# Optimization experiments

Measured on AMD Instinct MI355X. Metric: run time of the kernel, lower is better.

## Reference

```python
import jax, jax.numpy as jnp
import numpy as np

OFFSETS = (12, 20, 30, 42, 55, 67)  # pixel offsets along shadow direction


def _bilinear_shift(img, dx, dy):
    """Sample img (H,W) at (y+dy, x+dx), bilinear, zero padding.
    Equivalent to F.grid_sample with identity affine_grid + uniform shift
    (align_corners=True): normalized shift d*2/(W-1) == d pixels.
    Separable interpolation (valid because padding is zeros)."""
    H, W = img.shape
    xs = jnp.arange(W, dtype=img.dtype) + dx  # (W,) sample x-coords
    ys = jnp.arange(H, dtype=img.dtype) + dy  # (H,) sample y-coords
    x0f = jnp.floor(xs); wx = xs - x0f
    y0f = jnp.floor(ys); wy = ys - y0f
    x0 = x0f.astype(jnp.int32); x1 = x0 + 1
    y0 = y0f.astype(jnp.int32); y1 = y0 + 1

    def gx(ix):  # gather columns with zero padding
        valid = ((ix >= 0) & (ix < W)).astype(img.dtype)
        return img[:, jnp.clip(ix, 0, W - 1)] * valid[None, :]

    row = gx(x0) * (1.0 - wx)[None, :] + gx(x1) * wx[None, :]  # (H,W)

    def gy(iy):  # gather rows with zero padding
        valid = ((iy >= 0) & (iy < H)).astype(img.dtype)
        return row[jnp.clip(iy, 0, H - 1), :] * valid[:, None]

    return gy(y0) * (1.0 - wy)[:, None] + gy(y1) * wy[:, None]


def _warp_stack(shadow_map, shadow_dir):
    """shadow_map (B,1,H,W), shadow_dir (B,2) -> (B,n_offsets,H,W)."""
    img = shadow_map[:, 0]  # (B,H,W)
    d = jnp.asarray(OFFSETS, dtype=img.dtype)  # (n,)
    dx = shadow_dir[:, 0:1] * d          # (B,n) pixel shift in x
    dy = -shadow_dir[:, 1:2] * d         # (B,n) pixel shift in y
    f = jax.vmap(jax.vmap(_bilinear_shift, in_axes=(None, 0, 0)),
                 in_axes=(0, 0, 0))
    return f(img, dx, dy)  # (B,n,H,W)


def setup_inputs() -> dict:
    key = jax.random.key(0)
    k1, k2, k3, k4, k5 = jax.random.split(key, 5)
    B, C, Hf, Wf = 4, 512, 128, 128
    H, W = 1024, 1024
    n = len(OFFSETS)
    rgb_feat = jax.random.normal(k1, (B, C, Hf, Wf), dtype=jnp.float32)
    shadow_map = jax.random.uniform(k2, (B, 1, H, W), dtype=jnp.float32)
    shadow_dir = jax.random.normal(k3, (B, 2), dtype=jnp.float32)
    shadow_dir = shadow_dir / jnp.linalg.norm(shadow_dir, axis=-1, keepdims=True)
    w_conv = 0.02 * jax.random.normal(k4, (C, n), dtype=jnp.float32)
    b_conv = 0.02 * jax.random.normal(k5, (C,), dtype=jnp.float32)
    gate = jnp.ones((1,), dtype=jnp.float32) * 0.01
    return {"rgb_feat": rgb_feat, "shadow_map": shadow_map,
            "shadow_dir": shadow_dir, "w_conv": w_conv,
            "b_conv": b_conv, "gate": gate}


def reference(rgb_feat, shadow_map, shadow_dir, w_conv, b_conv, gate):
    B, C, Hf, Wf = rgb_feat.shape
    n = len(OFFSETS)
    evidence = _warp_stack(shadow_map, shadow_dir)  # (B,n,H,W)
    # bilinear downsample, align_corners=False, no antialias (matches torch)
    evidence = jax.image.resize(evidence, (B, n, Hf, Wf),
                                method="linear", antialias=False)
    mixed = jnp.einsum("bnhw,cn->bchw", evidence, w_conv) \
            + b_conv[None, :, None, None]
    return rgb_feat + gate[0] * mixed
```

## Files before the change

kernel.cpp:

```cpp
#include <hip/hip_runtime.h>

#define HRES 1024
#define WRES 1024
#define HF   128
#define WF   128
#define NOFF 6
#define CCH  512
#define BB   4
#define CHUNK 32

typedef float vfloat4 __attribute__((ext_vector_type(4)));
typedef vfloat4 uvfloat4 __attribute__((aligned(4)));

__global__ void evidence_kernel(const float* __restrict__ smap,
                                const float* __restrict__ sdir,
                                float* __restrict__ E) {
    int t = blockIdx.x * blockDim.x + threadIdx.x;
    if (t >= BB * NOFF * HF * WF) return;
    int j = t & (WF - 1);
    int i = (t >> 7) & (HF - 1);
    int k = (t >> 14) % NOFF;
    int b = t / (NOFF << 14);

    const float offs[NOFF] = {12.f, 20.f, 30.f, 42.f, 55.f, 67.f};
    float dirx = sdir[b * 2 + 0];
    float diry = sdir[b * 2 + 1];
    float d  = offs[k];
    float dx = dirx * d;
    float dy = -diry * d;
    float fxf = floorf(dx), fyf = floorf(dy);
    float wx = dx - fxf,    wy = dy - fyf;

    int X0 = 8 * j + 3 + (int)fxf;
    int Y0 = 8 * i + 3 + (int)fyf;

    float wx0 = 0.5f * (1.f - wx), wx1 = 0.5f, wx2 = 0.5f * wx;
    float wyv[3] = {0.5f * (1.f - wy), 0.5f, 0.5f * wy};

    const float* img = smap + (size_t)b * HRES * WRES;
    bool fastx = (X0 >= 0) & (X0 + 3 < WRES);
    float acc = 0.f;
#pragma unroll
    for (int r = 0; r < 3; ++r) {
        int y = Y0 + r;
        if ((unsigned)y < HRES) {
            const float* rowp = img + (size_t)y * WRES;
            float s0, s1, s2;
            if (fastx) {
                vfloat4 v = *reinterpret_cast<const uvfloat4*>(rowp + X0);
                s0 = v.x; s1 = v.y; s2 = v.z;
            } else {
                s0 = ((unsigned)(X0 + 0) < WRES) ? rowp[X0 + 0] : 0.f;
                s1 = ((unsigned)(X0 + 1) < WRES) ? rowp[X0 + 1] : 0.f;
                s2 = ((unsigned)(X0 + 2) < WRES) ? rowp[X0 + 2] : 0.f;
            }
            acc += (s0 * wx0 + s1 * wx1 + s2 * wx2) * wyv[r];
        }
    }
    E[t] = acc;
}

__global__ __launch_bounds__(256) void mix_kernel(
        const float* __restrict__ rgb,
        const float* __restrict__ E,
        const float* __restrict__ w_conv,
        const float* __restrict__ b_conv,
        const float* __restrict__ gate,
        float* __restrict__ out) {
    __shared__ float s_w[CHUNK * NOFF];
    __shared__ float s_b[CHUNK];

    int tile = blockIdx.x;
    int b    = tile >> 4;
    int p    = (tile & 15) * 1024 + threadIdx.x * 4;
    int c0   = blockIdx.y * CHUNK;
    float g  = gate[0];

    for (int idx = threadIdx.x; idx < CHUNK * NOFF; idx += blockDim.x)
        s_w[idx] = g * w_conv[(size_t)(c0 + idx / NOFF) * NOFF + idx % NOFF];
    for (int idx = threadIdx.x; idx < CHUNK; idx += blockDim.x)
        s_b[idx] = g * b_conv[c0 + idx];
    __syncthreads();

    vfloat4 e[NOFF];
#pragma unroll
    for (int k = 0; k < NOFF; ++k)
        e[k] = *reinterpret_cast<const vfloat4*>(
            E + (((size_t)(b * NOFF + k)) << 14) + p);

    const vfloat4* rgbp = reinterpret_cast<const vfloat4*>(
        rgb + (((size_t)(b * CCH + c0)) << 14) + p);
    vfloat4* outp = reinterpret_cast<vfloat4*>(
        out + (((size_t)(b * CCH + c0)) << 14) + p);
    const int stride4 = (1 << 14) / 4;

#pragma unroll
    for (int c8 = 0; c8 < CHUNK / 8; ++c8) {
        vfloat4 r[8];
#pragma unroll
        for (int u = 0; u < 8; ++u)
            r[u] = __builtin_nontemporal_load(
                rgbp + (size_t)(c8 * 8 + u) * stride4);
#pragma unroll
        for (int u = 0; u < 8; ++u) {
            int c = c8 * 8 + u;
            float w0 = s_w[c * NOFF + 0], w1 = s_w[c * NOFF + 1];
            float w2 = s_w[c * NOFF + 2], w3 = s_w[c * NOFF + 3];
            float w4 = s_w[c * NOFF + 4], w5 = s_w[c * NOFF + 5];
            float bb = s_b[c];
            vfloat4 o;
            o.x = r[u].x + bb + e[0].x * w0 + e[1].x * w1 + e[2].x * w2
                               + e[3].x * w3 + e[4].x * w4 + e[5].x * w5;
            o.y = r[u].y + bb + e[0].y * w0 + e[1].y * w1 + e[2].y * w2
                               + e[3].y * w3 + e[4].y * w4 + e[5].y * w5;
            o.z = r[u].z + bb + e[0].z * w0 + e[1].z * w1 + e[2].z * w2
                               + e[3].z * w3 + e[4].z * w4 + e[5].z * w5;
            o.w = r[u].w + bb + e[0].w * w0 + e[1].w * w1 + e[2].w * w2
                               + e[3].w * w3 + e[4].w * w4 + e[5].w * w5;
            __builtin_nontemporal_store(o, outp + (size_t)c * stride4);
        }
    }
}

extern "C" void kernel_launch(void* const* d_in, const int* in_sizes, int n_in,
                              void* d_out, int out_size, void* d_ws, size_t ws_size,
                              hipStream_t stream) {
    const float* rgb    = (const float*)d_in[0];
    const float* smap   = (const float*)d_in[1];
    const float* sdir   = (const float*)d_in[2];
    const float* w_conv = (const float*)d_in[3];
    const float* b_conv = (const float*)d_in[4];
    const float* gate   = (const float*)d_in[5];
    float* out = (float*)d_out;

    float* E = (float*)d_ws;
    int n_e = BB * NOFF * HF * WF;
    evidence_kernel<<<(n_e + 255) / 256, 256, 0, stream>>>(smap, sdir, E);

    dim3 grid_mix(BB * 16, CCH / CHUNK);
    mix_kernel<<<grid_mix, 256, 0, stream>>>(rgb, E, w_conv, b_conv, gate, out);
}
```

Before: 58.60 us.

## Remap evidence blocks for locality and drop shared-memory weight staging in mix

The evidence kernel now permutes block indices so that consecutively scheduled blocks work on neighbouring rows of the shadow map, aiming for better L2/cache reuse of the overlapping 3x3 row reads across XCDs. The mix kernel no longer stages gated weights and biases in shared memory behind a barrier. Instead it loads weights directly (scalar/uniform loads) and folds the gate into the evidence values once. This removes the LDS fill and __syncthreads, and the mix kernel is memory-bound on the rgb stream, so the gain is likely small.

```diff
diff --git a/kernel.cpp b/kernel.cpp
--- a/kernel.cpp
+++ b/kernel.cpp
@@ -15,8 +15,15 @@
 __global__ void evidence_kernel(const float* __restrict__ smap,
                                 const float* __restrict__ sdir,
                                 float* __restrict__ E) {
-    int t = blockIdx.x * blockDim.x + threadIdx.x;
-    if (t >= BB * NOFF * HF * WF) return;
+    int B = blockIdx.x;
+    int r   = B & 7;
+    int q   = B >> 3;
+    int b64 = q >> 3;
+    int sub = q & 7;
+    int off = 4 * r + sub + (sub >= 4 ? 28 : 0);
+    int c   = b64 * 64 + off;
+    int t   = c * 256 + threadIdx.x;
+
     int j = t & (WF - 1);
     int i = (t >> 7) & (HF - 1);
     int k = (t >> 14) % NOFF;
@@ -41,8 +48,8 @@
     bool fastx = (X0 >= 0) & (X0 + 3 < WRES);
     float acc = 0.f;
 #pragma unroll
-    for (int r = 0; r < 3; ++r) {
-        int y = Y0 + r;
+    for (int rr = 0; rr < 3; ++rr) {
+        int y = Y0 + rr;
         if ((unsigned)y < HRES) {
             const float* rowp = img + (size_t)y * WRES;
             float s0, s1, s2;
@@ -54,7 +61,7 @@
                 s1 = ((unsigned)(X0 + 1) < WRES) ? rowp[X0 + 1] : 0.f;
                 s2 = ((unsigned)(X0 + 2) < WRES) ? rowp[X0 + 2] : 0.f;
             }
-            acc += (s0 * wx0 + s1 * wx1 + s2 * wx2) * wyv[r];
+            acc += (s0 * wx0 + s1 * wx1 + s2 * wx2) * wyv[rr];
         }
     }
     E[t] = acc;
@@ -67,26 +74,19 @@
         const float* __restrict__ b_conv,
         const float* __restrict__ gate,
         float* __restrict__ out) {
-    __shared__ float s_w[CHUNK * NOFF];
-    __shared__ float s_b[CHUNK];
-
     int tile = blockIdx.x;
     int b    = tile >> 4;
     int p    = (tile & 15) * 1024 + threadIdx.x * 4;
     int c0   = blockIdx.y * CHUNK;
     float g  = gate[0];
 
-    for (int idx = threadIdx.x; idx < CHUNK * NOFF; idx += blockDim.x)
-        s_w[idx] = g * w_conv[(size_t)(c0 + idx / NOFF) * NOFF + idx % NOFF];
-    for (int idx = threadIdx.x; idx < CHUNK; idx += blockDim.x)
-        s_b[idx] = g * b_conv[c0 + idx];
-    __syncthreads();
-
     vfloat4 e[NOFF];
 #pragma unroll
-    for (int k = 0; k < NOFF; ++k)
+    for (int k = 0; k < NOFF; ++k) {
         e[k] = *reinterpret_cast<const vfloat4*>(
             E + (((size_t)(b * NOFF + k)) << 14) + p);
+        e[k] *= g;
+    }
 
     const vfloat4* rgbp = reinterpret_cast<const vfloat4*>(
         rgb + (((size_t)(b * CCH + c0)) << 14) + p);
@@ -96,26 +96,27 @@
 
 #pragma unroll
     for (int c8 = 0; c8 < CHUNK / 8; ++c8) {
-        vfloat4 r[8];
+        vfloat4 rv[8];
 #pragma unroll
         for (int u = 0; u < 8; ++u)
-            r[u] = __builtin_nontemporal_load(
+            rv[u] = __builtin_nontemporal_load(
                 rgbp + (size_t)(c8 * 8 + u) * stride4);
 #pragma unroll
         for (int u = 0; u < 8; ++u) {
-            int c = c8 * 8 + u;
-            float w0 = s_w[c * NOFF + 0], w1 = s_w[c * NOFF + 1];
-            float w2 = s_w[c * NOFF + 2], w3 = s_w[c * NOFF + 3];
-            float w4 = s_w[c * NOFF + 4], w5 = s_w[c * NOFF + 5];
-            float bb = s_b[c];
+            int c  = c8 * 8 + u;
+            int cg = c0 + c;
+            const float* wrow = w_conv + (size_t)cg * NOFF;
+            float w0 = wrow[0], w1 = wrow[1], w2 = wrow[2];
+            float w3 = wrow[3], w4 = wrow[4], w5 = wrow[5];
+            float bb = g * b_conv[cg];
             vfloat4 o;
-            o.x = r[u].x + bb + e[0].x * w0 + e[1].x * w1 + e[2].x * w2
+            o.x = rv[u].x + bb + e[0].x * w0 + e[1].x * w1 + e[2].x * w2
                                + e[3].x * w3 + e[4].x * w4 + e[5].x * w5;
-            o.y = r[u].y + bb + e[0].y * w0 + e[1].y * w1 + e[2].y * w2
+            o.y = rv[u].y + bb + e[0].y * w0 + e[1].y * w1 + e[2].y * w2
                                + e[3].y * w3 + e[4].y * w4 + e[5].y * w5;
-            o.z = r[u].z + bb + e[0].z * w0 + e[1].z * w1 + e[2].z * w2
+            o.z = rv[u].z + bb + e[0].z * w0 + e[1].z * w1 + e[2].z * w2
                                + e[3].z * w3 + e[4].z * w4 + e[5].z * w5;
-            o.w = r[u].w + bb + e[0].w * w0 + e[1].w * w1 + e[2].w * w2
+            o.w = rv[u].w + bb + e[0].w * w0 + e[1].w * w1 + e[2].w * w2
                                + e[3].w * w3 + e[4].w * w4 + e[5].w * w5;
             __builtin_nontemporal_store(o, outp + (size_t)c * stride4);
         }
@@ -134,8 +135,7 @@
     float* out = (float*)d_out;
 
     float* E = (float*)d_ws;
-    int n_e = BB * NOFF * HF * WF;
-    evidence_kernel<<<(n_e + 255) / 256, 256, 0, stream>>>(smap, sdir, E);
+    evidence_kernel<<<1536, 256, 0, stream>>>(smap, sdir, E);
 
     dim3 grid_mix(BB * 16, CCH / CHUNK);
     mix_kernel<<<grid_mix, 256, 0, stream>>>(rgb, E, w_conv, b_conv, gate, out);
```

After: 58.87 us. Within noise of the previous version (+0.5%).
